# Performance work log

Measured on AMD Instinct MI355X. Metric: run time of the kernel, lower is better.

Reference implementation:

```python
import jax, jax.numpy as jnp
import numpy as np

SDF_W = 7000.0
EIK_W = 600.0
ORI_W = 500.0
NEAR_ORI_W = 10.0
GRADN_W = 200.0
K_NEIGHBORS = 2


def _orientation_sign(query, surface, normals, k=K_NEIGHBORS):
    # Original detaches to numpy for a scipy KDTree query -> stop_gradient here.
    q = jax.lax.stop_gradient(query)       # [Q,3]
    s = jax.lax.stop_gradient(surface)     # [S,3]
    n = jax.lax.stop_gradient(normals)     # [S,3]
    # Brute-force squared distances [Q,S] (GEMM-dominated).
    d2 = (jnp.sum(q * q, axis=-1, keepdims=True)
          - 2.0 * (q @ s.T)
          + jnp.sum(s * s, axis=-1)[None, :])
    _, idx = jax.lax.top_k(-d2, k)         # [Q,k] nearest-neighbor indices
    near_pts = s[idx]                      # [Q,k,3]
    near_nrm = n[idx]                      # [Q,k,3]
    vecs = q[:, None, :] - near_pts        # [Q,k,3]
    dots = jnp.sum(vecs * near_nrm, axis=-1)  # [Q,k]
    return jnp.sign(jnp.mean(dots, axis=1))   # [Q]


def setup_inputs() -> dict:
    key = jax.random.key(0)
    ks = jax.random.split(key, 8)
    N = 16384
    return {
        "manifold_pred": jax.random.normal(ks[0], (N, 1), jnp.float32) * 0.1,
        "manifold_grad": jax.random.normal(ks[1], (N, 3), jnp.float32),
        "nonmanifold_pred": jax.random.normal(ks[2], (N, 1), jnp.float32),
        "near_points_pred": jax.random.normal(ks[3], (N, 1), jnp.float32) * 0.1,
        "surface_points": jax.random.normal(ks[4], (N, 3), jnp.float32),
        "surface_normals": jax.random.normal(ks[5], (N, 3), jnp.float32),
        "off_surface_points": jax.random.normal(ks[6], (N, 3), jnp.float32) * 1.5,
        "near_points": jax.random.normal(ks[7], (N, 3), jnp.float32),
    }


def reference(manifold_pred, manifold_grad, nonmanifold_pred, near_points_pred,
              surface_points, surface_normals, off_surface_points, near_points):
    sdf_loss = jnp.mean(manifold_pred ** 2)
    eikonal_loss = jnp.mean((jnp.linalg.norm(manifold_grad, axis=-1) - 1.0) ** 2)

    signs_off = _orientation_sign(off_surface_points, surface_points, surface_normals)
    orientation_loss = jnp.mean(jax.nn.relu(-nonmanifold_pred * signs_off[:, None]))

    signs_near = _orientation_sign(near_points, surface_points, surface_normals)
    near_surface_orientation_loss = jnp.mean(jax.nn.relu(-near_points_pred * signs_near[:, None]))

    gradient_normal_loss = jnp.mean((manifold_grad - surface_normals) ** 2)

    total = (SDF_W * sdf_loss + EIK_W * eikonal_loss + ORI_W * orientation_loss
             + NEAR_ORI_W * near_surface_orientation_loss + GRADN_W * gradient_normal_loss)
    return (total, sdf_loss, eikonal_loss, orientation_loss,
            near_surface_orientation_loss, gradient_normal_loss)
```

## Files before the change

### kernel.cpp

```cpp
#include <hip/hip_runtime.h>
#include <math.h>

#define SDF_W      7000.0f
#define EIK_W      600.0f
#define ORI_W      500.0f
#define NEAR_ORI_W 10.0f
#define GRADN_W    200.0f

#define TILE   2048
#define NWAVE  8
#define CHK    64
#define QPL    4
#define QB     (QPL * 64)
#define NSPLIT 4
#define WS_STRIDE 8192
#define WS_REC 65536


__device__ __forceinline__ float neg_half_norm2(float sx, float sy, float sz) {
    return -0.5f * fmaf(sx, sx, fmaf(sy, sy, sz * sz));
}
__device__ __forceinline__ float score(float qx, float qy, float qz,
                                       float sx, float sy, float sz, float nh) {
    return fmaf(qx, sx, fmaf(qy, sy, fmaf(qz, sz, nh)));
}

__device__ __forceinline__ float dot_at(const float* __restrict__ surf,
                                        const float* __restrict__ norms, int j,
                                        float qx, float qy, float qz) {
    float sx = surf[3*j], sy = surf[3*j+1], sz = surf[3*j+2];
    float nx = norms[3*j], ny = norms[3*j+1], nz = norms[3*j+2];
    return fmaf(qx - sx, nx, fmaf(qy - sy, ny, (qz - sz) * nz));
}

__global__ __launch_bounds__(512) void nn_scan(
    const float* __restrict__ offq, const float* __restrict__ nearq,
    const float* __restrict__ surf,
    float* __restrict__ ws, int S, int Qoff, int QT)
{
    __shared__ float4 tile[TILE];
    const int t    = threadIdx.x;
    const int lane = t & 63;
    const int wv   = __builtin_amdgcn_readfirstlane(t >> 6);

    const int qgroup = blockIdx.x >> 2;
    const int part   = blockIdx.x & 3;

    const int partLen = (((S + NSPLIT - 1) / NSPLIT) + (CHK - 1)) & ~(CHK - 1);
    int sb = part * partLen;       if (sb > S) sb = S;
    int se = sb + partLen;         if (se > S) se = S;

    const int qbase = qgroup * QB;
    float qx[QPL], qy[QPL], qz[QPL];
    #pragma unroll
    for (int j = 0; j < QPL; ++j) {
        int q = qbase + j * 64 + lane;
        qx[j] = 0.f; qy[j] = 0.f; qz[j] = 0.f;
        if (q < QT) {
            const float* p = (q < Qoff) ? (offq + 3 * q) : (nearq + 3 * (q - Qoff));
            qx[j] = p[0]; qy[j] = p[1]; qz[j] = p[2];
        }
    }

    float M1[QPL], M2[QPL], P1[QPL], P2[QPL];
    int c1[QPL], c2[QPL];
    #pragma unroll
    for (int j = 0; j < QPL; ++j) {
        M1[j] = -3.0e38f; M2[j] = -3.0e38f;
        P1[j] = -3.0e38f; P2[j] = -3.0e38f;
        c1[j] = 0; c2[j] = 0;
    }

    for (int base = sb; base < se; base += TILE) {
        __syncthreads();
        {
            int p0 = base + t * 4;
            if (p0 + 4 <= se) {
                const float4* g4 = (const float4*)(surf + 3 * p0);
                float4 r0 = g4[0], r1 = g4[1], r2 = g4[2];
                tile[t*4+0] = make_float4(r0.x, r0.y, r0.z, neg_half_norm2(r0.x, r0.y, r0.z));
                tile[t*4+1] = make_float4(r0.w, r1.x, r1.y, neg_half_norm2(r0.w, r1.x, r1.y));
                tile[t*4+2] = make_float4(r1.z, r1.w, r2.x, neg_half_norm2(r1.z, r1.w, r2.x));
                tile[t*4+3] = make_float4(r2.y, r2.z, r2.w, neg_half_norm2(r2.y, r2.z, r2.w));
            } else {
                #pragma unroll
                for (int k = 0; k < 4; ++k) {
                    int p = p0 + k;
                    if (p < se) {
                        float sx = surf[3*p], sy = surf[3*p+1], sz = surf[3*p+2];
                        tile[t*4+k] = make_float4(sx, sy, sz, neg_half_norm2(sx, sy, sz));
                    } else {
                        tile[t*4+k] = make_float4(0.f, 0.f, 0.f, -3.0e38f);
                    }
                }
            }
        }
        __syncthreads();
        const int lo = wv * (TILE / NWAVE);
        const float4* tp = tile + lo;
        const int ccbase = (base + lo) >> 6;
        #pragma unroll 1
        for (int c4 = 0; c4 < (TILE / NWAVE) / CHK; ++c4) {
            const float4* cp = tp + c4 * CHK;
            #pragma unroll 8
            for (int o = 0; o < CHK; ++o) {
                float4 s4 = cp[o];
                #pragma unroll
                for (int j = 0; j < QPL; ++j) {
                    float g = score(qx[j], qy[j], qz[j], s4.x, s4.y, s4.z, s4.w);
                    M2[j] = __builtin_amdgcn_fmed3f(g, M1[j], M2[j]);
                    M1[j] = fmaxf(M1[j], g);
                }
            }
            int cid = ccbase + c4;
            #pragma unroll
            for (int j = 0; j < QPL; ++j) {
                c1[j] = (M1[j] != P1[j]) ? cid : c1[j];  P1[j] = M1[j];
                c2[j] = (M2[j] != P2[j]) ? cid : c2[j];  P2[j] = M2[j];
            }
        }
    }

    __syncthreads();
    float4* rec = tile;
    #pragma unroll
    for (int j = 0; j < QPL; ++j)
        rec[wv * QB + j * 64 + lane] =
            make_float4(M1[j], M2[j], __int_as_float(c1[j]), __int_as_float(c2[j]));
    __syncthreads();
    if (t < QB) {
        float4 r = rec[t];
        float m1 = r.x, m2 = r.y;
        int k1 = __float_as_int(r.z), k2 = __float_as_int(r.w);
        #pragma unroll
        for (int w = 1; w < NWAVE; ++w) {
            float4 a = rec[w * QB + t];
            float a1 = a.x, a2 = a.y;
            int ac1 = __float_as_int(a.z), ac2 = __float_as_int(a.w);
            if (a1 > m1)      { m2 = m1; k2 = k1; m1 = a1; k1 = ac1; }
            else if (a1 > m2) { m2 = a1; k2 = ac1; }
            if (a2 > m2)      { m2 = a2; k2 = ac2; }
        }
        int gq = qbase + t;
        if (gq < QT) {
            ((float4*)(ws + WS_REC))[gq * NSPLIT + part] =
                make_float4(m1, m2, __int_as_float(k1), __int_as_float(k2));
        }
    }
}

__global__ __launch_bounds__(512) void recover_k(
    const float* __restrict__ offq, const float* __restrict__ nearq,
    const float* __restrict__ surf, const float* __restrict__ norms,
    const float* __restrict__ nmpred, const float* __restrict__ nppred,
    const float* __restrict__ mp, const float* __restrict__ mg,
    const float* __restrict__ sn,
    float* __restrict__ ws, int S, int Qoff, int QT, int N)
{
    const int t    = threadIdx.x;
    const int lane = t & 63;
    const int wv   = t >> 6;
    const int q    = blockIdx.x * 8 + wv;

    float termOri = 0.f, termNori = 0.f;
    if (q < QT) {
        const float4* recs = (const float4*)(ws + WS_REC);
        float M1 = -3.0e38f, M2 = -3.0e38f;
        int c1 = 0, c2 = 0;
        #pragma unroll
        for (int h = 0; h < NSPLIT; ++h) {
            float4 r = recs[q * NSPLIT + h];
            float a1 = r.x, a2 = r.y;
            int ac1 = __float_as_int(r.z), ac2 = __float_as_int(r.w);
            if (a1 > M1)      { M2 = M1; c2 = c1; M1 = a1; c1 = ac1; }
            else if (a1 > M2) { M2 = a1; c2 = ac1; }
            if (a2 > M2)      { M2 = a2; c2 = ac2; }
        }
        bool isNear = (q >= Qoff);
        const float* qp = isNear ? (nearq + 3 * (q - Qoff)) : (offq + 3 * q);
        float qx = qp[0], qy = qp[1], qz = qp[2];

        int j1 = c1 * CHK + lane;
        float g1 = -3.0e38f, dot1 = 0.f;
        if (j1 < S) {
            float sx = surf[3*j1], sy = surf[3*j1+1], sz = surf[3*j1+2];
            g1 = score(qx, qy, qz, sx, sy, sz, neg_half_norm2(sx, sy, sz));
            float nx = norms[3*j1], ny = norms[3*j1+1], nz = norms[3*j1+2];
            dot1 = fmaf(qx - sx, nx, fmaf(qy - sy, ny, (qz - sz) * nz));
        }
        unsigned long long m1mask = __ballot(g1 == M1);
        int I1; float d1;
        if (m1mask) {
            int l1 = __ffsll(m1mask) - 1;
            I1 = c1 * CHK + l1;
            d1 = __shfl(dot1, l1);
        } else {
            I1 = 0;
            d1 = dot_at(surf, norms, 0, qx, qy, qz);
        }

        int j2 = c2 * CHK + lane;
        float g2 = -3.0e38f, dot2 = 0.f;
        if (j2 < S) {
            float sx = surf[3*j2], sy = surf[3*j2+1], sz = surf[3*j2+2];
            g2 = score(qx, qy, qz, sx, sy, sz, neg_half_norm2(sx, sy, sz));
            float nx = norms[3*j2], ny = norms[3*j2+1], nz = norms[3*j2+2];
            dot2 = fmaf(qx - sx, nx, fmaf(qy - sy, ny, (qz - sz) * nz));
        }
        unsigned long long m2mask = __ballot(g2 == M2);
        int rel = I1 - c2 * CHK;
        if (rel >= 0 && rel < 64) m2mask &= ~(1ull << rel);
        int I2; float d2;
        if (m2mask) {
            int l2 = __ffsll(m2mask) - 1;
            I2 = c2 * CHK + l2;
            d2 = __shfl(dot2, l2);
        } else {
            I2 = (I1 == 0 && S > 1) ? 1 : 0;
            d2 = dot_at(surf, norms, I2, qx, qy, qz);
        }

        float ms = d1 + d2;
        float sgn = (ms > 0.f) ? 1.f : ((ms < 0.f) ? -1.f : 0.f);
        float pred = isNear ? nppred[q - Qoff] : nmpred[q];
        float term = fmaxf(0.f, -pred * sgn);
        if (lane == 0) {
            termOri  = isNear ? 0.f : term;
            termNori = isNear ? term : 0.f;
        }
    }

    float sdf = 0.f, eik = 0.f, gn = 0.f;
    for (int i = blockIdx.x * 512 + t; i < N; i += gridDim.x * 512) {
        float p = mp[i];
        sdf += p * p;
        float gx = mg[3*i], gy = mg[3*i+1], gz = mg[3*i+2];
        float nrm = sqrtf(fmaf(gx, gx, fmaf(gy, gy, gz * gz)));
        float d = nrm - 1.0f;
        eik += d * d;
        float nx = sn[3*i], ny = sn[3*i+1], nz = sn[3*i+2];
        float dx = gx - nx, dy = gy - ny, dz = gz - nz;
        gn += fmaf(dx, dx, fmaf(dy, dy, dz * dz));
    }

    float v0 = termOri, v1 = termNori, v2 = sdf, v3 = eik, v4 = gn;
    #pragma unroll
    for (int off = 32; off > 0; off >>= 1) {
        v0 += __shfl_down(v0, off);
        v1 += __shfl_down(v1, off);
        v2 += __shfl_down(v2, off);
        v3 += __shfl_down(v3, off);
        v4 += __shfl_down(v4, off);
    }
    __shared__ float red[5][NWAVE];
    if (lane == 0) {
        red[0][wv] = v0; red[1][wv] = v1; red[2][wv] = v2;
        red[3][wv] = v3; red[4][wv] = v4;
    }
    __syncthreads();
    if (t == 0) {
        #pragma unroll
        for (int k = 0; k < 5; ++k) {
            float s = 0.f;
            #pragma unroll
            for (int w = 0; w < NWAVE; ++w) s += red[k][w];
            ws[k * WS_STRIDE + blockIdx.x] = s;
        }
    }
}

__global__ __launch_bounds__(256) void final_k(
    const float* __restrict__ ws, float* __restrict__ out,
    int N, int RB, int Qoff, int Qnear)
{
    __shared__ float r[5][256];
    int t = threadIdx.x;
    float s[5] = {0.f, 0.f, 0.f, 0.f, 0.f};
    for (int i = t; i < RB; i += 256) {
        #pragma unroll
        for (int k = 0; k < 5; ++k) s[k] += ws[k * WS_STRIDE + i];
    }
    #pragma unroll
    for (int k = 0; k < 5; ++k) r[k][t] = s[k];
    __syncthreads();
    for (int off = 128; off > 0; off >>= 1) {
        if (t < off) {
            #pragma unroll
            for (int k = 0; k < 5; ++k) r[k][t] += r[k][t + off];
        }
        __syncthreads();
    }
    if (t == 0) {
        float orim  = r[0][0] / (float)Qoff;
        float norim = r[1][0] / (float)Qnear;
        float sdfm  = r[2][0] / (float)N;
        float eikm  = r[3][0] / (float)N;
        float gnm   = r[4][0] / (3.0f * (float)N);
        out[0] = SDF_W * sdfm + EIK_W * eikm + ORI_W * orim
               + NEAR_ORI_W * norim + GRADN_W * gnm;
        out[1] = sdfm;
        out[2] = eikm;
        out[3] = orim;
        out[4] = norim;
        out[5] = gnm;
    }
}

extern "C" void kernel_launch(void* const* d_in, const int* in_sizes, int n_in,
                              void* d_out, int out_size, void* d_ws, size_t ws_size,
                              hipStream_t stream)
{
    const float* mp    = (const float*)d_in[0];
    const float* mg    = (const float*)d_in[1];
    const float* nmp   = (const float*)d_in[2];
    const float* npp   = (const float*)d_in[3];
    const float* sp    = (const float*)d_in[4];
    const float* sn    = (const float*)d_in[5];
    const float* offp  = (const float*)d_in[6];
    const float* nearp = (const float*)d_in[7];
    float* out = (float*)d_out;

    const int N     = in_sizes[0];
    const int S     = in_sizes[4] / 3;
    const int Qoff  = in_sizes[2];
    const int Qnear = in_sizes[3];
    const int QT    = Qoff + Qnear;

    float* ws = (float*)d_ws;

    const int qgroups = (QT + QB - 1) / QB;
    const int RB      = (QT + 7) / 8;

    nn_scan<<<qgroups * NSPLIT, 512, 0, stream>>>(offp, nearp, sp, ws, S, Qoff, QT);
    recover_k<<<RB, 512, 0, stream>>>(offp, nearp, sp, sn, nmp, npp,
                                      mp, mg, sn, ws, S, Qoff, QT, N);
    final_k<<<1, 256, 0, stream>>>(ws, out, N, RB, Qoff, Qnear);
}
```

Measured before the change: 160.4 us.

## Double queries per lane, split surface eight ways, batch recover per wave

Raises queries per lane from 4 to 8 and the surface split from 4 to 8 parts, so each loaded surface point is reused across more queries while the grid size stays the same. The cross-wave reduction is reworked into two halves so the larger per-block record still fits in the shared tile. The recover kernel now handles 8 queries per wave with both neighbour-chunk loads issued together, cutting its block count. The cost is higher register pressure under the new occupancy bound, less inner-loop unrolling, and twice as many partial records to merge.

```diff
diff --git a/kernel.cpp b/kernel.cpp
--- a/kernel.cpp
+++ b/kernel.cpp
@@ -10,9 +10,10 @@
 #define TILE   2048
 #define NWAVE  8
 #define CHK    64
-#define QPL    4
+#define QPL    8
 #define QB     (QPL * 64)
-#define NSPLIT 4
+#define NSPLIT 8
+#define QPW    8
 #define WS_STRIDE 8192
 #define WS_REC 65536
 
@@ -33,7 +34,7 @@
     return fmaf(qx - sx, nx, fmaf(qy - sy, ny, (qz - sz) * nz));
 }
 
-__global__ __launch_bounds__(512) void nn_scan(
+__global__ __launch_bounds__(512, 4) void nn_scan(
     const float* __restrict__ offq, const float* __restrict__ nearq,
     const float* __restrict__ surf,
     float* __restrict__ ws, int S, int Qoff, int QT)
@@ -43,8 +44,8 @@
     const int lane = t & 63;
     const int wv   = __builtin_amdgcn_readfirstlane(t >> 6);
 
-    const int qgroup = blockIdx.x >> 2;
-    const int part   = blockIdx.x & 3;
+    const int qgroup = blockIdx.x >> 3;
+    const int part   = blockIdx.x & 7;
 
     const int partLen = (((S + NSPLIT - 1) / NSPLIT) + (CHK - 1)) & ~(CHK - 1);
     int sb = part * partLen;       if (sb > S) sb = S;
@@ -102,7 +103,7 @@
         #pragma unroll 1
         for (int c4 = 0; c4 < (TILE / NWAVE) / CHK; ++c4) {
             const float4* cp = tp + c4 * CHK;
-            #pragma unroll 8
+            #pragma unroll 2
             for (int o = 0; o < CHK; ++o) {
                 float4 s4 = cp[o];
                 #pragma unroll
@@ -123,29 +124,45 @@
 
     __syncthreads();
     float4* rec = tile;
-    #pragma unroll
-    for (int j = 0; j < QPL; ++j)
-        rec[wv * QB + j * 64 + lane] =
-            make_float4(M1[j], M2[j], __int_as_float(c1[j]), __int_as_float(c2[j]));
-    __syncthreads();
-    if (t < QB) {
-        float4 r = rec[t];
-        float m1 = r.x, m2 = r.y;
-        int k1 = __float_as_int(r.z), k2 = __float_as_int(r.w);
-        #pragma unroll
-        for (int w = 1; w < NWAVE; ++w) {
-            float4 a = rec[w * QB + t];
-            float a1 = a.x, a2 = a.y;
-            int ac1 = __float_as_int(a.z), ac2 = __float_as_int(a.w);
-            if (a1 > m1)      { m2 = m1; k2 = k1; m1 = a1; k1 = ac1; }
-            else if (a1 > m2) { m2 = a1; k2 = ac1; }
-            if (a2 > m2)      { m2 = a2; k2 = ac2; }
-        }
-        int gq = qbase + t;
-        if (gq < QT) {
-            ((float4*)(ws + WS_REC))[gq * NSPLIT + part] =
-                make_float4(m1, m2, __int_as_float(k1), __int_as_float(k2));
-        }
+    if (wv < 4) {
+        #pragma unroll
+        for (int j = 0; j < QPL; ++j)
+            rec[wv * QB + j * 64 + lane] =
+                make_float4(M1[j], M2[j], __int_as_float(c1[j]), __int_as_float(c2[j]));
+    }
+    __syncthreads();
+    float m1 = -3.0e38f, m2 = -3.0e38f;
+    int k1 = 0, k2 = 0;
+    #pragma unroll
+    for (int w = 0; w < 4; ++w) {
+        float4 a = rec[w * QB + t];
+        float a1 = a.x, a2 = a.y;
+        int ac1 = __float_as_int(a.z), ac2 = __float_as_int(a.w);
+        if (a1 > m1)      { m2 = m1; k2 = k1; m1 = a1; k1 = ac1; }
+        else if (a1 > m2) { m2 = a1; k2 = ac1; }
+        if (a2 > m2)      { m2 = a2; k2 = ac2; }
+    }
+    __syncthreads();
+    if (wv >= 4) {
+        #pragma unroll
+        for (int j = 0; j < QPL; ++j)
+            rec[(wv - 4) * QB + j * 64 + lane] =
+                make_float4(M1[j], M2[j], __int_as_float(c1[j]), __int_as_float(c2[j]));
+    }
+    __syncthreads();
+    #pragma unroll
+    for (int w = 0; w < 4; ++w) {
+        float4 a = rec[w * QB + t];
+        float a1 = a.x, a2 = a.y;
+        int ac1 = __float_as_int(a.z), ac2 = __float_as_int(a.w);
+        if (a1 > m1)      { m2 = m1; k2 = k1; m1 = a1; k1 = ac1; }
+        else if (a1 > m2) { m2 = a1; k2 = ac1; }
+        if (a2 > m2)      { m2 = a2; k2 = ac2; }
+    }
+    int gq = qbase + t;
+    if (gq < QT) {
+        ((float4*)(ws + WS_REC))[gq * NSPLIT + part] =
+            make_float4(m1, m2, __int_as_float(k1), __int_as_float(k2));
     }
 }
 
@@ -160,11 +177,15 @@
     const int t    = threadIdx.x;
     const int lane = t & 63;
     const int wv   = t >> 6;
-    const int q    = blockIdx.x * 8 + wv;
-
-    float termOri = 0.f, termNori = 0.f;
-    if (q < QT) {
-        const float4* recs = (const float4*)(ws + WS_REC);
+
+    float accOri = 0.f, accNori = 0.f;
+    const int q0 = (blockIdx.x * NWAVE + wv) * QPW;
+    const float4* recs = (const float4*)(ws + WS_REC);
+
+    for (int u = 0; u < QPW; ++u) {
+        int q = q0 + u;
+        if (q >= QT) break;
+
         float M1 = -3.0e38f, M2 = -3.0e38f;
         int c1 = 0, c2 = 0;
         #pragma unroll
@@ -181,13 +202,21 @@
         float qx = qp[0], qy = qp[1], qz = qp[2];
 
         int j1 = c1 * CHK + lane;
-        float g1 = -3.0e38f, dot1 = 0.f;
+        int j2 = c2 * CHK + lane;
+        float g1 = -3.0e38f, dot1 = 0.f, g2 = -3.0e38f, dot2 = 0.f;
         if (j1 < S) {
             float sx = surf[3*j1], sy = surf[3*j1+1], sz = surf[3*j1+2];
+            float nx = norms[3*j1], ny = norms[3*j1+1], nz = norms[3*j1+2];
             g1 = score(qx, qy, qz, sx, sy, sz, neg_half_norm2(sx, sy, sz));
-            float nx = norms[3*j1], ny = norms[3*j1+1], nz = norms[3*j1+2];
             dot1 = fmaf(qx - sx, nx, fmaf(qy - sy, ny, (qz - sz) * nz));
         }
+        if (j2 < S) {
+            float sx = surf[3*j2], sy = surf[3*j2+1], sz = surf[3*j2+2];
+            float nx = norms[3*j2], ny = norms[3*j2+1], nz = norms[3*j2+2];
+            g2 = score(qx, qy, qz, sx, sy, sz, neg_half_norm2(sx, sy, sz));
+            dot2 = fmaf(qx - sx, nx, fmaf(qy - sy, ny, (qz - sz) * nz));
+        }
+
         unsigned long long m1mask = __ballot(g1 == M1);
         int I1; float d1;
         if (m1mask) {
@@ -199,24 +228,15 @@
             d1 = dot_at(surf, norms, 0, qx, qy, qz);
         }
 
-        int j2 = c2 * CHK + lane;
-        float g2 = -3.0e38f, dot2 = 0.f;
-        if (j2 < S) {
-            float sx = surf[3*j2], sy = surf[3*j2+1], sz = surf[3*j2+2];
-            g2 = score(qx, qy, qz, sx, sy, sz, neg_half_norm2(sx, sy, sz));
-            float nx = norms[3*j2], ny = norms[3*j2+1], nz = norms[3*j2+2];
-            dot2 = fmaf(qx - sx, nx, fmaf(qy - sy, ny, (qz - sz) * nz));
-        }
         unsigned long long m2mask = __ballot(g2 == M2);
         int rel = I1 - c2 * CHK;
         if (rel >= 0 && rel < 64) m2mask &= ~(1ull << rel);
-        int I2; float d2;
+        float d2;
         if (m2mask) {
             int l2 = __ffsll(m2mask) - 1;
-            I2 = c2 * CHK + l2;
             d2 = __shfl(dot2, l2);
         } else {
-            I2 = (I1 == 0 && S > 1) ? 1 : 0;
+            int I2 = (I1 == 0 && S > 1) ? 1 : 0;
             d2 = dot_at(surf, norms, I2, qx, qy, qz);
         }
 
@@ -225,8 +245,7 @@
         float pred = isNear ? nppred[q - Qoff] : nmpred[q];
         float term = fmaxf(0.f, -pred * sgn);
         if (lane == 0) {
-            termOri  = isNear ? 0.f : term;
-            termNori = isNear ? term : 0.f;
+            if (isNear) accNori += term; else accOri += term;
         }
     }
 
@@ -243,7 +262,7 @@
         gn += fmaf(dx, dx, fmaf(dy, dy, dz * dz));
     }
 
-    float v0 = termOri, v1 = termNori, v2 = sdf, v3 = eik, v4 = gn;
+    float v0 = accOri, v1 = accNori, v2 = sdf, v3 = eik, v4 = gn;
     #pragma unroll
     for (int off = 32; off > 0; off >>= 1) {
         v0 += __shfl_down(v0, off);
@@ -329,10 +348,10 @@
     float* ws = (float*)d_ws;
 
     const int qgroups = (QT + QB - 1) / QB;
-    const int RB      = (QT + 7) / 8;
+    const int RBLK    = (QT + NWAVE * QPW - 1) / (NWAVE * QPW);
 
     nn_scan<<<qgroups * NSPLIT, 512, 0, stream>>>(offp, nearp, sp, ws, S, Qoff, QT);
-    recover_k<<<RB, 512, 0, stream>>>(offp, nearp, sp, sn, nmp, npp,
-                                      mp, mg, sn, ws, S, Qoff, QT, N);
-    final_k<<<1, 256, 0, stream>>>(ws, out, N, RB, Qoff, Qnear);
-}
+    recover_k<<<RBLK, 512, 0, stream>>>(offp, nearp, sp, sn, nmp, npp,
+                                        mp, mg, sn, ws, S, Qoff, QT, N);
+    final_k<<<1, 256, 0, stream>>>(ws, out, N, RBLK, Qoff, Qnear);
+}
```

Measured after the change: 166.3 us. 1.04x slower.
